# Kernel optimization log

Measured on AMD Instinct MI355X. Metric: run time of the kernel, lower is better.

The kernel has to match this reference:

```python
import jax, jax.numpy as jnp
import numpy as np

D_MODEL = 512
D_INNER = 1024   # expand=2
D_STATE = 16
D_CONV = 4
DT_RANK = 32     # ceil(d_model/16)
N_LAYERS = 3
STATE_DIM = 256
NUM_ACTIONS = 9
BATCH = 8
SEQ = 1024


def setup_inputs() -> dict:
    key = jax.random.key(0)
    ks = iter(jax.random.split(key, 32))
    def nrm(shape, scale=0.02):
        return jax.random.normal(next(ks), shape, jnp.float32) * scale
    inp = {}
    inp["state_sequences"] = jax.random.normal(next(ks), (BATCH, SEQ, STATE_DIM), jnp.float32)
    inp["embed_w"] = nrm((D_MODEL, STATE_DIM), STATE_DIM ** -0.5)
    inp["embed_b"] = jnp.zeros((D_MODEL,), jnp.float32)
    inp["in_proj_w"] = nrm((N_LAYERS, 2 * D_INNER, D_MODEL), D_MODEL ** -0.5)
    inp["conv_w"] = nrm((N_LAYERS, D_INNER, D_CONV), 0.2)
    inp["conv_b"] = jnp.zeros((N_LAYERS, D_INNER), jnp.float32)
    inp["x_proj_w"] = nrm((N_LAYERS, DT_RANK + 2 * D_STATE, D_INNER), D_INNER ** -0.5)
    inp["dt_proj_w"] = nrm((N_LAYERS, D_INNER, DT_RANK), DT_RANK ** -0.5)
    # bias so that softplus(dt) ~ 0.01 (standard mamba dt init)
    inp["dt_proj_b"] = jnp.full((N_LAYERS, D_INNER), float(np.log(np.expm1(0.01))), jnp.float32)
    # S4D-real init: A_n = n for n = 1..d_state
    inp["A_log"] = jnp.log(jnp.broadcast_to(
        jnp.arange(1, D_STATE + 1, dtype=jnp.float32), (N_LAYERS, D_INNER, D_STATE)))
    inp["D"] = jnp.ones((N_LAYERS, D_INNER), jnp.float32)
    inp["out_proj_w"] = nrm((N_LAYERS, D_MODEL, D_INNER), D_INNER ** -0.5)
    inp["head1_w"] = nrm((D_MODEL // 2, D_MODEL), D_MODEL ** -0.5)
    inp["head1_b"] = jnp.zeros((D_MODEL // 2,), jnp.float32)
    inp["head2_w"] = nrm((NUM_ACTIONS, D_MODEL // 2), (D_MODEL // 2) ** -0.5)
    inp["head2_b"] = jnp.zeros((NUM_ACTIONS,), jnp.float32)
    return inp


def _mamba_block(x, in_w, cw, cb, xw, dtw, dtb, A_log, Dp, ow):
    """One mamba-ssm Mamba layer (d_inner=2*d_model, d_state=16, d_conv=4)."""
    B, L, _ = x.shape
    xz = jnp.einsum('bld,ed->ble', x, in_w)            # (B,L,2*d_inner)
    xi, z = jnp.split(xz, 2, axis=-1)
    # causal depthwise conv1d along time
    xc = jnp.pad(xi, ((0, 0), (D_CONV - 1, 0), (0, 0)))
    conv = jax.lax.conv_general_dilated(
        xc.transpose(0, 2, 1), cw[:, None, :], (1,), 'VALID',
        feature_group_count=D_INNER)                   # (B,d_inner,L)
    xi = jax.nn.silu(conv.transpose(0, 2, 1) + cb)     # (B,L,d_inner)
    dbl = jnp.einsum('bld,ed->ble', xi, xw)            # (B,L,dt_rank+2*d_state)
    dt, Bm, Cm = jnp.split(dbl, [DT_RANK, DT_RANK + D_STATE], axis=-1)
    dt = jax.nn.softplus(jnp.einsum('blr,dr->bld', dt, dtw) + dtb)  # (B,L,d_inner)
    A = -jnp.exp(A_log)                                # (d_inner,d_state)

    def step(h, inputs):
        dt_t, x_t, B_t, C_t = inputs                   # (B,di),(B,di),(B,ds),(B,ds)
        dA = jnp.exp(dt_t[:, :, None] * A)             # (B,di,ds)
        h = dA * h + (dt_t * x_t)[:, :, None] * B_t[:, None, :]
        y_t = jnp.einsum('bds,bs->bd', h, C_t)
        return h, y_t

    h0 = jnp.zeros((B, D_INNER, D_STATE), xi.dtype)
    seq = (dt.transpose(1, 0, 2), xi.transpose(1, 0, 2),
           Bm.transpose(1, 0, 2), Cm.transpose(1, 0, 2))
    _, ys = jax.lax.scan(step, h0, seq)                # (L,B,d_inner)
    y = ys.transpose(1, 0, 2) + xi * Dp
    y = y * jax.nn.silu(z)
    return jnp.einsum('bld,ed->ble', y, ow)            # (B,L,d_model)


def reference(state_sequences, embed_w, embed_b, in_proj_w, conv_w, conv_b,
              x_proj_w, dt_proj_w, dt_proj_b, A_log, D, out_proj_w,
              head1_w, head1_b, head2_w, head2_b):
    x = jnp.einsum('bls,ds->bld', state_sequences, embed_w) + embed_b
    for i in range(N_LAYERS):
        x = _mamba_block(x, in_proj_w[i], conv_w[i], conv_b[i], x_proj_w[i],
                         dt_proj_w[i], dt_proj_b[i], A_log[i], D[i], out_proj_w[i])
    h = jax.nn.relu(jnp.einsum('bd,hd->bh', x[:, -1, :], head1_w) + head1_b)
    logits = jnp.einsum('bh,ah->ba', h, head2_w) + head2_b  # (B,num_actions)
    return logits
```

## Files before the change

### kernel.cpp

```cpp
#include <hip/hip_runtime.h>
#include <cstdint>
#include <cstddef>


#define DEVI static __device__ __forceinline__

using short8 = __attribute__((ext_vector_type(8))) short;
using f32x4  = __attribute__((ext_vector_type(4))) float;
typedef unsigned short ushort;
typedef unsigned int uint;

DEVI float sigmoidf_(float x) { return 1.f / (1.f + __expf(-x)); }
DEVI float siluf_(float x)    { return x * sigmoidf_(x); }
DEVI float softplusf_(float x){ return fmaxf(x, 0.f) + log1pf(expf(-fabsf(x))); }

DEVI ushort rne_bf16(float f) {
    uint u = __float_as_uint(f);
    return (ushort)((u + 0x7fffu + ((u >> 16) & 1u)) >> 16);
}
DEVI float bf16_to_f(ushort h) { return __uint_as_float(((uint)h) << 16); }

constexpr int LC = 32;
constexpr int NC = 32;
constexpr int PF = 8;

DEVI void cvt4(const float4 v, ushort* h, ushort* l) {
    const float vv[4] = {v.x, v.y, v.z, v.w};
    #pragma unroll
    for (int e = 0; e < 4; e++) {
        const ushort hh = rne_bf16(vv[e]);
        h[e] = hh;
        l[e] = rne_bf16(vv[e] - bf16_to_f(hh));
    }
}

__global__ __launch_bounds__(256)
void wcvt_kernel(const float* __restrict__ src, ushort* __restrict__ hi,
                 ushort* __restrict__ lo, int n4)
{
    const int idx = blockIdx.x * 256 + threadIdx.x;
    if (idx >= n4) return;
    const float4 v = reinterpret_cast<const float4*>(src)[idx];
    ushort h[4], l[4];
    cvt4(v, h, l);
    *reinterpret_cast<ushort4*>(&hi[idx * 4]) = make_ushort4(h[0], h[1], h[2], h[3]);
    *reinterpret_cast<ushort4*>(&lo[idx * 4]) = make_ushort4(l[0], l[1], l[2], l[3]);
}

__global__ __launch_bounds__(256)
void wcvt3_kernel(const float* __restrict__ s_in, const float* __restrict__ s_out,
                  const float* __restrict__ s_xp, ushort* __restrict__ dst)
{
    const int idx = blockIdx.x * 256 + threadIdx.x;
    if (idx >= 409600) return;
    const int e0 = idx * 4;
    const float* src; ushort* hb; ushort* lb; int loc;
    if (e0 < 1048576)      { src = s_in;  hb = dst;           lb = dst + 1048576; loc = e0; }
    else if (e0 < 1572864) { src = s_out; hb = dst + 2097152; lb = dst + 2621440; loc = e0 - 1048576; }
    else                   { src = s_xp;  hb = dst + 3145728; lb = dst + 3211264; loc = e0 - 1572864; }
    const float4 v = *reinterpret_cast<const float4*>(&src[loc]);
    ushort h[4], l[4];
    cvt4(v, h, l);
    *reinterpret_cast<ushort4*>(&hb[loc]) = make_ushort4(h[0], h[1], h[2], h[3]);
    *reinterpret_cast<ushort4*>(&lb[loc]) = make_ushort4(l[0], l[1], l[2], l[3]);
}

template<int ACT>
__global__ __launch_bounds__(256)
void gemm_mfma(const float* __restrict__ A, int lda,
               const ushort* __restrict__ Whi, const ushort* __restrict__ Wlo,
               int ldw, const float* __restrict__ bias,
               float* __restrict__ C, int ldc, int K)
{
    __shared__ short As_hi[4096], As_lo[4096], Ws_hi[4096], Ws_lo[4096];

    const int tid  = threadIdx.x;
    const int lane = tid & 63;
    const int wave = tid >> 6;
    const int wr   = wave >> 1;
    const int wc   = wave & 1;
    const int row0 = blockIdx.y * 128;
    const int col0 = blockIdx.x * 128;

    const int g  = tid & 3;
    const int r0 = tid >> 2;

    const int lg = lane >> 4;
    const int lm = lane & 15;
    const int chA = lg * 128 + ((wr * 64 + lm) ^ lg);
    const int chB = lg * 128 + ((wc * 64 + lm) ^ lg);

    f32x4 acc[4][4];
    #pragma unroll
    for (int i = 0; i < 4; i++)
        #pragma unroll
        for (int j = 0; j < 4; j++) acc[i][j] = (f32x4){0.f, 0.f, 0.f, 0.f};

    float4 av0[2], av1[2];
    short8 wh[2], wl8[2];

    auto gload = [&](int k0) {
        #pragma unroll
        for (int p = 0; p < 2; p++) {
            const int rr = r0 + p * 64;
            const float* ap = A + (size_t)(row0 + rr) * lda + k0 + g * 8;
            av0[p] = *reinterpret_cast<const float4*>(ap);
            av1[p] = *reinterpret_cast<const float4*>(ap + 4);
            const size_t wo = (size_t)(col0 + rr) * ldw + k0 + g * 8;
            wh[p]  = *reinterpret_cast<const short8*>(&Whi[wo]);
            wl8[p] = *reinterpret_cast<const short8*>(&Wlo[wo]);
        }
    };

    gload(0);

    for (int k0 = 0; k0 < K; k0 += 32) {
        #pragma unroll
        for (int p = 0; p < 2; p++) {
            const int ch = g * 128 + ((r0 + p * 64) ^ g);
            ushort h[8], l[8];
            cvt4(av0[p], h, l);
            cvt4(av1[p], h + 4, l + 4);
            short8 h8, l8;
            #pragma unroll
            for (int e = 0; e < 8; e++) { h8[e] = (short)h[e]; l8[e] = (short)l[e]; }
            *reinterpret_cast<short8*>(&As_hi[ch * 8]) = h8;
            *reinterpret_cast<short8*>(&As_lo[ch * 8]) = l8;
            *reinterpret_cast<short8*>(&Ws_hi[ch * 8]) = wh[p];
            *reinterpret_cast<short8*>(&Ws_lo[ch * 8]) = wl8[p];
        }
        if (k0 + 32 < K) gload(k0 + 32);
        __syncthreads();

        short8 a_hi[4], a_lo[4], b_hi[4], b_lo[4];
        #pragma unroll
        for (int i = 0; i < 4; i++) {
            a_hi[i] = *reinterpret_cast<const short8*>(&As_hi[(chA + i * 16) * 8]);
            a_lo[i] = *reinterpret_cast<const short8*>(&As_lo[(chA + i * 16) * 8]);
        }
        #pragma unroll
        for (int j = 0; j < 4; j++) {
            b_hi[j] = *reinterpret_cast<const short8*>(&Ws_hi[(chB + j * 16) * 8]);
            b_lo[j] = *reinterpret_cast<const short8*>(&Ws_lo[(chB + j * 16) * 8]);
        }
        #pragma unroll
        for (int i = 0; i < 4; i++)
            #pragma unroll
            for (int j = 0; j < 4; j++) {
                acc[i][j] = __builtin_amdgcn_mfma_f32_16x16x32_bf16(a_hi[i], b_hi[j], acc[i][j], 0, 0, 0);
                acc[i][j] = __builtin_amdgcn_mfma_f32_16x16x32_bf16(a_hi[i], b_lo[j], acc[i][j], 0, 0, 0);
                acc[i][j] = __builtin_amdgcn_mfma_f32_16x16x32_bf16(a_lo[i], b_hi[j], acc[i][j], 0, 0, 0);
            }
        __syncthreads();
    }

    #pragma unroll
    for (int i = 0; i < 4; i++) {
        const int grow = row0 + wr * 64 + i * 16 + lg * 4;
        #pragma unroll
        for (int j = 0; j < 4; j++) {
            const int gcol = col0 + wc * 64 + j * 16 + lm;
            float bv = 0.f;
            if constexpr (ACT >= 1) bv = bias[gcol];
            #pragma unroll
            for (int r = 0; r < 4; r++)
                C[(size_t)(grow + r) * ldc + gcol] = acc[i][j][r] + bv;
        }
    }
}

__global__ __launch_bounds__(256)
void gemm_mfma_xp(const float* __restrict__ A,
                  const ushort* __restrict__ Whi,
                  const ushort* __restrict__ Wlo,
                  float* __restrict__ P)
{
    __shared__ short As_hi[2048], As_lo[2048], Ws_hi[2048], Ws_lo[2048];

    const int tid  = threadIdx.x;
    const int lane = tid & 63;
    const int wave = tid >> 6;
    const int wr   = wave >> 1;
    const int wc   = wave & 1;
    const int row0 = blockIdx.x * 64;
    const int kp   = blockIdx.y;

    const int g = tid & 3;
    const int r = tid >> 2;
    const int ch_st = g * 64 + (r ^ g);

    const int lg = lane >> 4;
    const int lm = lane & 15;

    f32x4 acc[2][2];
    #pragma unroll
    for (int i = 0; i < 2; i++)
        #pragma unroll
        for (int j = 0; j < 2; j++) acc[i][j] = (f32x4){0.f, 0.f, 0.f, 0.f};

    for (int ks = 0; ks < 4; ks++) {
        const int kbase = kp * 128 + ks * 32;
        __syncthreads();
        {
            const float* ap = A + (size_t)(row0 + r) * 1024 + kbase + g * 8;
            const float4 v0 = *reinterpret_cast<const float4*>(ap);
            const float4 v1 = *reinterpret_cast<const float4*>(ap + 4);
            ushort h[8], l[8];
            cvt4(v0, h, l);
            cvt4(v1, h + 4, l + 4);
            short8 h8, l8;
            #pragma unroll
            for (int e = 0; e < 8; e++) { h8[e] = (short)h[e]; l8[e] = (short)l[e]; }
            *reinterpret_cast<short8*>(&As_hi[ch_st * 8]) = h8;
            *reinterpret_cast<short8*>(&As_lo[ch_st * 8]) = l8;
        }
        {
            const size_t wo = (size_t)r * 1024 + kbase + g * 8;
            *reinterpret_cast<short8*>(&Ws_hi[ch_st * 8]) =
                *reinterpret_cast<const short8*>(&Whi[wo]);
            *reinterpret_cast<short8*>(&Ws_lo[ch_st * 8]) =
                *reinterpret_cast<const short8*>(&Wlo[wo]);
        }
        __syncthreads();

        short8 a_hi[2], a_lo[2], b_hi[2], b_lo[2];
        #pragma unroll
        for (int i = 0; i < 2; i++) {
            const int ch = lg * 64 + ((wr * 32 + i * 16 + lm) ^ lg);
            a_hi[i] = *reinterpret_cast<const short8*>(&As_hi[ch * 8]);
            a_lo[i] = *reinterpret_cast<const short8*>(&As_lo[ch * 8]);
        }
        #pragma unroll
        for (int j = 0; j < 2; j++) {
            const int ch = lg * 64 + ((wc * 32 + j * 16 + lm) ^ lg);
            b_hi[j] = *reinterpret_cast<const short8*>(&Ws_hi[ch * 8]);
            b_lo[j] = *reinterpret_cast<const short8*>(&Ws_lo[ch * 8]);
        }
        #pragma unroll
        for (int i = 0; i < 2; i++)
            #pragma unroll
            for (int j = 0; j < 2; j++) {
                acc[i][j] = __builtin_amdgcn_mfma_f32_16x16x32_bf16(a_hi[i], b_hi[j], acc[i][j], 0, 0, 0);
                acc[i][j] = __builtin_amdgcn_mfma_f32_16x16x32_bf16(a_hi[i], b_lo[j], acc[i][j], 0, 0, 0);
                acc[i][j] = __builtin_amdgcn_mfma_f32_16x16x32_bf16(a_lo[i], b_hi[j], acc[i][j], 0, 0, 0);
            }
    }

    #pragma unroll
    for (int i = 0; i < 2; i++) {
        const int grow = row0 + wr * 32 + i * 16 + lg * 4;
        #pragma unroll
        for (int j = 0; j < 2; j++) {
            const int gcol = wc * 32 + j * 16 + lm;
            #pragma unroll
            for (int rr = 0; rr < 4; rr++)
                P[((size_t)kp * 8192 + grow + rr) * 64 + gcol] = acc[i][j][rr];
        }
    }
}

__global__ __launch_bounds__(256)
void xp_reduce(const float* __restrict__ P, float* __restrict__ dbl)
{
    const int idx = blockIdx.x * 256 + threadIdx.x;
    float s = 0.f;
    #pragma unroll
    for (int p = 0; p < 8; p++) s += P[(size_t)p * 524288 + idx];
    dbl[idx] = s;
}

__global__ __launch_bounds__(256)
void conv_silu_kernel(const float* __restrict__ xz,
                      const float* __restrict__ cw,
                      const float* __restrict__ cb,
                      float* __restrict__ xi)
{
    const int idx = blockIdx.x * 256 + threadIdx.x;
    const int d = idx & 1023;
    const int l = (idx >> 10) & 1023;
    const int b = idx >> 20;

    const float4 w = reinterpret_cast<const float4*>(cw)[d];
    float acc = cb[d];
    const float* base = xz + (size_t)b * 1024 * 2048 + d;
    if (l >= 3) acc = fmaf(base[(size_t)(l - 3) * 2048], w.x, acc);
    if (l >= 2) acc = fmaf(base[(size_t)(l - 2) * 2048], w.y, acc);
    if (l >= 1) acc = fmaf(base[(size_t)(l - 1) * 2048], w.z, acc);
    acc = fmaf(base[(size_t)l * 2048], w.w, acc);
    xi[idx] = siluf_(acc);
}

__global__ __launch_bounds__(256)
void dt_kernel(const float* __restrict__ dbl,
               const float* __restrict__ dtw,
               const float* __restrict__ dtb,
               float* __restrict__ dtout)
{
    __shared__ float S[LC][32];
    const int tid = threadIdx.x;
    const int d   = blockIdx.x * 256 + tid;
    const int c   = blockIdx.y;
    const int b   = blockIdx.z;
    const int t0  = c * LC;

    {
        const int t = tid >> 3, q = tid & 7;
        *reinterpret_cast<float4*>(&S[t][q * 4]) =
            *reinterpret_cast<const float4*>(&dbl[((size_t)b * 1024 + t0 + t) * 64 + q * 4]);
    }
    __syncthreads();

    float W[32];
    #pragma unroll
    for (int q = 0; q < 8; q++)
        *reinterpret_cast<float4*>(&W[q * 4]) =
            *reinterpret_cast<const float4*>(&dtw[(size_t)d * 32 + q * 4]);
    const float bias = dtb[d];

    float* dto = dtout + ((size_t)b * 1024 + t0) * 1024 + d;
    #pragma unroll 4
    for (int t = 0; t < LC; t++) {
        float a0 = bias, a1 = 0.f, a2 = 0.f, a3 = 0.f;
        #pragma unroll
        for (int q = 0; q < 8; q += 4) {
            const float4 s0 = *reinterpret_cast<const float4*>(&S[t][q * 4]);
            const float4 s1 = *reinterpret_cast<const float4*>(&S[t][q * 4 + 4]);
            a0 = fmaf(W[q*4+0], s0.x, a0); a1 = fmaf(W[q*4+1], s0.y, a1);
            a2 = fmaf(W[q*4+2], s0.z, a2); a3 = fmaf(W[q*4+3], s0.w, a3);
            a0 = fmaf(W[q*4+4], s1.x, a0); a1 = fmaf(W[q*4+5], s1.y, a1);
            a2 = fmaf(W[q*4+6], s1.z, a2); a3 = fmaf(W[q*4+7], s1.w, a3);
        }
        dto[(size_t)t * 1024] = softplusf_((a0 + a1) + (a2 + a3));
    }
}

__global__ __launch_bounds__(256)
void scan_p1(const float* __restrict__ xi,
             const float* __restrict__ dtin,
             const float* __restrict__ dbl,
             const float* __restrict__ A_log,
             float* __restrict__ hend,
             float* __restrict__ dtsum)
{
    __shared__ float S[LC][16];
    const int tid = threadIdx.x;
    const int d   = blockIdx.x * 256 + tid;
    const int c   = blockIdx.y;
    const int b   = blockIdx.z;
    const int t0  = c * LC;

    if (tid < 128) {
        const int t = tid >> 2, q = tid & 3;
        *reinterpret_cast<float4*>(&S[t][q * 4]) =
            *reinterpret_cast<const float4*>(&dbl[((size_t)b * 1024 + t0 + t) * 64 + 32 + q * 4]);
    }
    __syncthreads();

    float A[16], h[16];
    #pragma unroll
    for (int s = 0; s < 16; s++) A[s] = -__expf(A_log[d * 16 + s]);
    #pragma unroll
    for (int s = 0; s < 16; s++) h[s] = 0.f;
    float dts = 0.f;

    const float* xi_p = xi   + ((size_t)b * 1024 + t0) * 1024 + d;
    const float* dt_p = dtin + ((size_t)b * 1024 + t0) * 1024 + d;

    float xA[PF], xB[PF], dA[PF], dB[PF];
    #pragma unroll
    for (int j = 0; j < PF; j++) {
        xA[j] = xi_p[(size_t)j * 1024];
        dA[j] = dt_p[(size_t)j * 1024];
    }

    auto batch = [&](int bt, float (&cx)[PF], float (&cd)[PF],
                     float (&nx)[PF], float (&nd)[PF], bool pre) {
        if (pre) {
            #pragma unroll
            for (int j = 0; j < PF; j++) {
                const size_t tt = (size_t)((bt + 1) * PF + j);
                nx[j] = xi_p[tt * 1024];
                nd[j] = dt_p[tt * 1024];
            }
        }
        #pragma unroll
        for (int j = 0; j < PF; j++) {
            const int t = bt * PF + j;
            const float dtv = cd[j];
            dts += dtv;
            const float dx = dtv * cx[j];
            #pragma unroll
            for (int q = 0; q < 4; q++) {
                const float4 Bv = *reinterpret_cast<const float4*>(&S[t][q * 4]);
                h[q*4+0] = fmaf(__expf(dtv * A[q*4+0]), h[q*4+0], dx * Bv.x);
                h[q*4+1] = fmaf(__expf(dtv * A[q*4+1]), h[q*4+1], dx * Bv.y);
                h[q*4+2] = fmaf(__expf(dtv * A[q*4+2]), h[q*4+2], dx * Bv.z);
                h[q*4+3] = fmaf(__expf(dtv * A[q*4+3]), h[q*4+3], dx * Bv.w);
            }
        }
    };
    batch(0, xA, dA, xB, dB, true);
    batch(1, xB, dB, xA, dA, true);
    batch(2, xA, dA, xB, dB, true);
    batch(3, xB, dB, xA, dA, false);

    float* hp = hend + (((size_t)b * NC + c) * 1024 + d) * 16;
    #pragma unroll
    for (int s = 0; s < 16; s += 4)
        *reinterpret_cast<float4*>(&hp[s]) = *reinterpret_cast<const float4*>(&h[s]);
    dtsum[((size_t)b * NC + c) * 1024 + d] = dts;
}

__global__ __launch_bounds__(256)
void scan_p2(float* __restrict__ hbuf,
             const float* __restrict__ dtsum,
             const float* __restrict__ A_log)
{
    const int gid = blockIdx.x * 256 + threadIdx.x;
    const int s = gid & 15;
    const int d = (gid >> 4) & 1023;
    const int b = gid >> 14;

    const float A = -__expf(A_log[d * 16 + s]);
    float h = 0.f;
    #pragma unroll
    for (int c = 0; c < NC; c++) {
        const size_t idx = (((size_t)b * NC + c) * 1024 + d) * 16 + s;
        const float he = hbuf[idx];
        const float aP = __expf(A * dtsum[((size_t)b * NC + c) * 1024 + d]);
        hbuf[idx] = h;
        h = fmaf(aP, h, he);
    }
}

__global__ __launch_bounds__(256)
void scan_p3(const float* __restrict__ xi,
             const float* __restrict__ dtin,
             const float* __restrict__ dbl,
             float* __restrict__ xz,
             const float* __restrict__ A_log,
             const float* __restrict__ Dp,
             const float* __restrict__ h0)
{
    __shared__ float S[LC][32];
    const int tid = threadIdx.x;
    const int d   = blockIdx.x * 256 + tid;
    const int c   = blockIdx.y;
    const int b   = blockIdx.z;
    const int t0  = c * LC;

    {
        const int t = tid >> 3, q = tid & 7;
        *reinterpret_cast<float4*>(&S[t][q * 4]) =
            *reinterpret_cast<const float4*>(&dbl[((size_t)b * 1024 + t0 + t) * 64 + 32 + q * 4]);
    }
    __syncthreads();

    float A[16], h[16];
    #pragma unroll
    for (int s = 0; s < 16; s++) A[s] = -__expf(A_log[d * 16 + s]);
    const float* h0p = h0 + (((size_t)b * NC + c) * 1024 + d) * 16;
    #pragma unroll
    for (int s = 0; s < 16; s += 4)
        *reinterpret_cast<float4*>(&h[s]) = *reinterpret_cast<const float4*>(&h0p[s]);

    const float Dv = Dp[d];
    const float* xi_p = xi   + ((size_t)b * 1024 + t0) * 1024 + d;
    const float* dt_p = dtin + ((size_t)b * 1024 + t0) * 1024 + d;
    const float* z_p  = xz   + ((size_t)b * 1024 + t0) * 2048 + 1024 + d;
    float*       y_p  = xz   + ((size_t)b * 1024 + t0) * 2048 + d;

    float xA[PF], xB[PF], zA[PF], zB[PF], dA[PF], dB[PF];
    #pragma unroll
    for (int j = 0; j < PF; j++) {
        xA[j] = xi_p[(size_t)j * 1024];
        zA[j] = z_p[(size_t)j * 2048];
        dA[j] = dt_p[(size_t)j * 1024];
    }

    auto batch = [&](int bt, float (&cx)[PF], float (&cz)[PF], float (&cd)[PF],
                     float (&nx)[PF], float (&nz)[PF], float (&nd)[PF], bool pre) {
        if (pre) {
            #pragma unroll
            for (int j = 0; j < PF; j++) {
                const size_t tt = (size_t)((bt + 1) * PF + j);
                nx[j] = xi_p[tt * 1024];
                nz[j] = z_p[tt * 2048];
                nd[j] = dt_p[tt * 1024];
            }
        }
        #pragma unroll
        for (int j = 0; j < PF; j++) {
            const int t = bt * PF + j;
            const float dtv = cd[j];
            const float dx  = dtv * cx[j];
            float y = 0.f;
            #pragma unroll
            for (int q = 0; q < 4; q++) {
                const float4 Bv = *reinterpret_cast<const float4*>(&S[t][q * 4]);
                const float4 Cv = *reinterpret_cast<const float4*>(&S[t][16 + q * 4]);
                h[q*4+0] = fmaf(__expf(dtv * A[q*4+0]), h[q*4+0], dx * Bv.x);
                h[q*4+1] = fmaf(__expf(dtv * A[q*4+1]), h[q*4+1], dx * Bv.y);
                h[q*4+2] = fmaf(__expf(dtv * A[q*4+2]), h[q*4+2], dx * Bv.z);
                h[q*4+3] = fmaf(__expf(dtv * A[q*4+3]), h[q*4+3], dx * Bv.w);
                y = fmaf(h[q*4+0], Cv.x, y);
                y = fmaf(h[q*4+1], Cv.y, y);
                y = fmaf(h[q*4+2], Cv.z, y);
                y = fmaf(h[q*4+3], Cv.w, y);
            }
            y_p[(size_t)t * 2048] = (y + cx[j] * Dv) * siluf_(cz[j]);
        }
    };
    batch(0, xA, zA, dA, xB, zB, dB, true);
    batch(1, xB, zB, dB, xA, zA, dA, true);
    batch(2, xA, zA, dA, xB, zB, dB, true);
    batch(3, xB, zB, dB, xA, zA, dA, false);
}

__global__ __launch_bounds__(256)
void head1_kernel(const float* __restrict__ x,
                  const float* __restrict__ w,
                  const float* __restrict__ bias,
                  float* __restrict__ hh)
{
    const int tid = threadIdx.x;
    const int jl  = tid >> 4;
    const int ks  = tid & 15;
    const int j   = blockIdx.x * 16 + jl;

    const float* wr = w + (size_t)j * 512 + ks * 32;
    float acc[8];
    #pragma unroll
    for (int b = 0; b < 8; b++) {
        const float* xr = x + ((size_t)b * 1024 + 1023) * 512 + ks * 32;
        float a = 0.f;
        #pragma unroll
        for (int k = 0; k < 32; k += 4) {
            const float4 wv = *reinterpret_cast<const float4*>(&wr[k]);
            const float4 xv = *reinterpret_cast<const float4*>(&xr[k]);
            a = fmaf(wv.x, xv.x, a); a = fmaf(wv.y, xv.y, a);
            a = fmaf(wv.z, xv.z, a); a = fmaf(wv.w, xv.w, a);
        }
        acc[b] = a;
    }
    #pragma unroll
    for (int b = 0; b < 8; b++) {
        float p = acc[b];
        p += __shfl_xor(p, 1);
        p += __shfl_xor(p, 2);
        p += __shfl_xor(p, 4);
        p += __shfl_xor(p, 8);
        if (ks == 0) hh[b * 256 + j] = fmaxf(p + bias[j], 0.f);
    }
}

__global__ void head2_kernel(const float* __restrict__ hh,
                             const float* __restrict__ w,
                             const float* __restrict__ b2,
                             float* __restrict__ out)
{
    const int t = threadIdx.x;
    if (t < 72) {
        const int bb = t / 9, a = t % 9;
        const float* hr = hh + bb * 256;
        const float* wr = w + a * 256;
        float acc = b2[a];
        for (int jj = 0; jj < 256; jj++) acc = fmaf(hr[jj], wr[jj], acc);
        out[t] = acc;
    }
}


extern "C" void kernel_launch(void* const* d_in, const int* in_sizes, int n_in,
                              void* d_out, int out_size, void* d_ws, size_t ws_size,
                              hipStream_t stream)
{
    const float* state     = (const float*)d_in[0];
    const float* embed_w   = (const float*)d_in[1];
    const float* embed_b   = (const float*)d_in[2];
    const float* in_proj_w = (const float*)d_in[3];
    const float* conv_w    = (const float*)d_in[4];
    const float* conv_b    = (const float*)d_in[5];
    const float* x_proj_w  = (const float*)d_in[6];
    const float* dt_proj_w = (const float*)d_in[7];
    const float* dt_proj_b = (const float*)d_in[8];
    const float* A_log     = (const float*)d_in[9];
    const float* Dp        = (const float*)d_in[10];
    const float* out_proj_w= (const float*)d_in[11];
    const float* h1w       = (const float*)d_in[12];
    const float* h1b       = (const float*)d_in[13];
    const float* h2w       = (const float*)d_in[14];
    const float* h2b       = (const float*)d_in[15];
    float* out = (float*)d_out;

    float* x    = (float*)d_ws;
    float* xz   = x    + (size_t)8192 * 512;
    float* xi   = xz   + (size_t)8192 * 2048;
    float* dtbf = xi   + (size_t)8192 * 1024;
    float* dbl  = dtbf + (size_t)8192 * 1024;
    float* hh   = dbl  + (size_t)8192 * 64;
    ushort* wl = (ushort*)(hh + 2048);
    ushort* we_hi = wl + 3276800;
    ushort* we_lo = we_hi + 131072;
    float* dtsum = (float*)(we_lo + 131072);

    float* dblp = x;
    float* hbuf = x;

    const dim3 blk(256);

    wcvt_kernel<<<dim3(128), blk, 0, stream>>>(embed_w, we_hi, we_lo, 131072 / 4);
    gemm_mfma<1><<<dim3(4, 64), blk, 0, stream>>>(
        state, 256, we_hi, we_lo, 256, embed_b, x, 512, 256);

    for (int i = 0; i < 3; i++) {
        const float* Alog_i = A_log + (size_t)i * 1024 * 16;
        const float* dtw_i  = dt_proj_w + (size_t)i * 1024 * 32;
        const float* dtb_i  = dt_proj_b + (size_t)i * 1024;

        wcvt3_kernel<<<dim3(1600), blk, 0, stream>>>(
            in_proj_w + (size_t)i * 2048 * 512,
            out_proj_w + (size_t)i * 512 * 1024,
            x_proj_w + (size_t)i * 64 * 1024, wl);

        gemm_mfma<0><<<dim3(16, 64), blk, 0, stream>>>(
            x, 512, wl, wl + 1048576, 512, nullptr, xz, 2048, 512);

        conv_silu_kernel<<<dim3(8 * 1024 * 1024 / 256), blk, 0, stream>>>(
            xz, conv_w + (size_t)i * 1024 * 4, conv_b + (size_t)i * 1024, xi);

        gemm_mfma_xp<<<dim3(128, 8), blk, 0, stream>>>(
            xi, wl + 3145728, wl + 3211264, dblp);
        xp_reduce<<<dim3(2048), blk, 0, stream>>>(dblp, dbl);

        dt_kernel<<<dim3(4, NC, 8), blk, 0, stream>>>(dbl, dtw_i, dtb_i, dtbf);

        scan_p1<<<dim3(4, NC, 8), blk, 0, stream>>>(
            xi, dtbf, dbl, Alog_i, hbuf, dtsum);
        scan_p2<<<dim3(512), blk, 0, stream>>>(hbuf, dtsum, Alog_i);
        scan_p3<<<dim3(4, NC, 8), blk, 0, stream>>>(
            xi, dtbf, dbl, xz, Alog_i, Dp + (size_t)i * 1024, hbuf);

        gemm_mfma<0><<<dim3(4, 64), blk, 0, stream>>>(
            xz, 2048, wl + 2097152, wl + 2621440, 1024, nullptr, x, 512, 1024);
    }

    head1_kernel<<<dim3(16), blk, 0, stream>>>(x, h1w, h1b, hh);
    head2_kernel<<<dim3(1), dim3(128), 0, stream>>>(hh, h2w, h2b, out);
}
```

Baseline: 834.9 us.

## Emit pre-split bf16 hi/lo activations from producers to skip GEMM-side conversion

Producers of the GEMM A operands (the embed GEMM, the out_proj GEMM and scan_p3) now write activations directly as bf16 hi/lo pairs instead of fp32. The consuming GEMMs load these split halves straight into shared memory and no longer run the per-tile fp32-to-bf16x2 conversion. Global traffic stays about the same size but the conversion ALU work is removed from the GEMM main loops. The head kernel is adapted to rebuild fp32 from the hi/lo pair. Buffer aliasing changes, with y stored inside the xz rows using a stride of 4096.

```diff
diff --git a/kernel.cpp b/kernel.cpp
--- a/kernel.cpp
+++ b/kernel.cpp
@@ -65,12 +65,15 @@
     *reinterpret_cast<ushort4*>(&lb[loc]) = make_ushort4(l[0], l[1], l[2], l[3]);
 }
 
-template<int ACT>
-__global__ __launch_bounds__(256)
-void gemm_mfma(const float* __restrict__ A, int lda,
+template<int ACT, bool ASPLIT, bool OSPLIT>
+__global__ __launch_bounds__(256)
+void gemm_mfma(const float* __restrict__ A,
+               const ushort* __restrict__ Ahi, const ushort* __restrict__ Alo,
+               int lda,
                const ushort* __restrict__ Whi, const ushort* __restrict__ Wlo,
                int ldw, const float* __restrict__ bias,
-               float* __restrict__ C, int ldc, int K)
+               float* __restrict__ C, ushort* __restrict__ Chi,
+               ushort* __restrict__ Clo, int ldc, int K)
 {
     __shared__ short As_hi[4096], As_lo[4096], Ws_hi[4096], Ws_lo[4096];
 
@@ -97,15 +100,21 @@
         for (int j = 0; j < 4; j++) acc[i][j] = (f32x4){0.f, 0.f, 0.f, 0.f};
 
     float4 av0[2], av1[2];
-    short8 wh[2], wl8[2];
+    short8 ah[2], al[2], wh[2], wl8[2];
 
     auto gload = [&](int k0) {
         #pragma unroll
         for (int p = 0; p < 2; p++) {
             const int rr = r0 + p * 64;
-            const float* ap = A + (size_t)(row0 + rr) * lda + k0 + g * 8;
-            av0[p] = *reinterpret_cast<const float4*>(ap);
-            av1[p] = *reinterpret_cast<const float4*>(ap + 4);
+            if constexpr (ASPLIT) {
+                const size_t ao = (size_t)(row0 + rr) * lda + k0 + g * 8;
+                ah[p] = *reinterpret_cast<const short8*>(&Ahi[ao]);
+                al[p] = *reinterpret_cast<const short8*>(&Alo[ao]);
+            } else {
+                const float* ap = A + (size_t)(row0 + rr) * lda + k0 + g * 8;
+                av0[p] = *reinterpret_cast<const float4*>(ap);
+                av1[p] = *reinterpret_cast<const float4*>(ap + 4);
+            }
             const size_t wo = (size_t)(col0 + rr) * ldw + k0 + g * 8;
             wh[p]  = *reinterpret_cast<const short8*>(&Whi[wo]);
             wl8[p] = *reinterpret_cast<const short8*>(&Wlo[wo]);
@@ -118,14 +127,19 @@
         #pragma unroll
         for (int p = 0; p < 2; p++) {
             const int ch = g * 128 + ((r0 + p * 64) ^ g);
-            ushort h[8], l[8];
-            cvt4(av0[p], h, l);
-            cvt4(av1[p], h + 4, l + 4);
-            short8 h8, l8;
-            #pragma unroll
-            for (int e = 0; e < 8; e++) { h8[e] = (short)h[e]; l8[e] = (short)l[e]; }
-            *reinterpret_cast<short8*>(&As_hi[ch * 8]) = h8;
-            *reinterpret_cast<short8*>(&As_lo[ch * 8]) = l8;
+            if constexpr (ASPLIT) {
+                *reinterpret_cast<short8*>(&As_hi[ch * 8]) = ah[p];
+                *reinterpret_cast<short8*>(&As_lo[ch * 8]) = al[p];
+            } else {
+                ushort h[8], l[8];
+                cvt4(av0[p], h, l);
+                cvt4(av1[p], h + 4, l + 4);
+                short8 h8, l8;
+                #pragma unroll
+                for (int e = 0; e < 8; e++) { h8[e] = (short)h[e]; l8[e] = (short)l[e]; }
+                *reinterpret_cast<short8*>(&As_hi[ch * 8]) = h8;
+                *reinterpret_cast<short8*>(&As_lo[ch * 8]) = l8;
+            }
             *reinterpret_cast<short8*>(&Ws_hi[ch * 8]) = wh[p];
             *reinterpret_cast<short8*>(&Ws_lo[ch * 8]) = wl8[p];
         }
@@ -163,8 +177,16 @@
             float bv = 0.f;
             if constexpr (ACT >= 1) bv = bias[gcol];
             #pragma unroll
-            for (int r = 0; r < 4; r++)
-                C[(size_t)(grow + r) * ldc + gcol] = acc[i][j][r] + bv;
+            for (int r = 0; r < 4; r++) {
+                const float v = acc[i][j][r] + bv;
+                if constexpr (OSPLIT) {
+                    const ushort hv = rne_bf16(v);
+                    Chi[(size_t)(grow + r) * ldc + gcol] = hv;
+                    Clo[(size_t)(grow + r) * ldc + gcol] = rne_bf16(v - bf16_to_f(hv));
+                } else {
+                    C[(size_t)(grow + r) * ldc + gcol] = v;
+                }
+            }
         }
     }
 }
@@ -468,7 +490,8 @@
     const float* xi_p = xi   + ((size_t)b * 1024 + t0) * 1024 + d;
     const float* dt_p = dtin + ((size_t)b * 1024 + t0) * 1024 + d;
     const float* z_p  = xz   + ((size_t)b * 1024 + t0) * 2048 + 1024 + d;
-    float*       y_p  = xz   + ((size_t)b * 1024 + t0) * 2048 + d;
+    ushort* yh_p = reinterpret_cast<ushort*>(xz + ((size_t)b * 1024 + t0) * 2048) + d;
+    ushort* yl_p = yh_p + 1024;
 
     float xA[PF], xB[PF], zA[PF], zB[PF], dA[PF], dB[PF];
     #pragma unroll
@@ -508,7 +531,10 @@
                 y = fmaf(h[q*4+2], Cv.z, y);
                 y = fmaf(h[q*4+3], Cv.w, y);
             }
-            y_p[(size_t)t * 2048] = (y + cx[j] * Dv) * siluf_(cz[j]);
+            const float yv = (y + cx[j] * Dv) * siluf_(cz[j]);
+            const ushort hv = rne_bf16(yv);
+            yh_p[(size_t)t * 4096] = hv;
+            yl_p[(size_t)t * 4096] = rne_bf16(yv - bf16_to_f(hv));
         }
     };
     batch(0, xA, zA, dA, xB, zB, dB, true);
@@ -518,7 +544,8 @@
 }
 
 __global__ __launch_bounds__(256)
-void head1_kernel(const float* __restrict__ x,
+void head1_kernel(const ushort* __restrict__ xh,
+                  const ushort* __restrict__ xl,
                   const float* __restrict__ w,
                   const float* __restrict__ bias,
                   float* __restrict__ hh)
@@ -532,14 +559,17 @@
     float acc[8];
     #pragma unroll
     for (int b = 0; b < 8; b++) {
-        const float* xr = x + ((size_t)b * 1024 + 1023) * 512 + ks * 32;
+        const size_t ro = ((size_t)b * 1024 + 1023) * 512 + ks * 32;
         float a = 0.f;
         #pragma unroll
         for (int k = 0; k < 32; k += 4) {
             const float4 wv = *reinterpret_cast<const float4*>(&wr[k]);
-            const float4 xv = *reinterpret_cast<const float4*>(&xr[k]);
-            a = fmaf(wv.x, xv.x, a); a = fmaf(wv.y, xv.y, a);
-            a = fmaf(wv.z, xv.z, a); a = fmaf(wv.w, xv.w, a);
+            const ushort4 hv = *reinterpret_cast<const ushort4*>(&xh[ro + k]);
+            const ushort4 lv = *reinterpret_cast<const ushort4*>(&xl[ro + k]);
+            a = fmaf(wv.x, bf16_to_f(hv.x) + bf16_to_f(lv.x), a);
+            a = fmaf(wv.y, bf16_to_f(hv.y) + bf16_to_f(lv.y), a);
+            a = fmaf(wv.z, bf16_to_f(hv.z) + bf16_to_f(lv.z), a);
+            a = fmaf(wv.w, bf16_to_f(hv.w) + bf16_to_f(lv.w), a);
         }
         acc[b] = a;
     }
@@ -593,8 +623,13 @@
     const float* h2b       = (const float*)d_in[15];
     float* out = (float*)d_out;
 
-    float* x    = (float*)d_ws;
-    float* xz   = x    + (size_t)8192 * 512;
+    float* reg0 = (float*)d_ws;
+    ushort* xh  = (ushort*)reg0;
+    ushort* xl  = xh + (size_t)8192 * 512;
+    float* dblp = reg0;
+    float* hbuf = reg0;
+
+    float* xz   = reg0 + (size_t)8192 * 512;
     float* xi   = xz   + (size_t)8192 * 2048;
     float* dtbf = xi   + (size_t)8192 * 1024;
     float* dbl  = dtbf + (size_t)8192 * 1024;
@@ -604,14 +639,15 @@
     ushort* we_lo = we_hi + 131072;
     float* dtsum = (float*)(we_lo + 131072);
 
-    float* dblp = x;
-    float* hbuf = x;
+    ushort* yh = (ushort*)xz;
+    ushort* yl = (ushort*)xz + 1024;
 
     const dim3 blk(256);
 
     wcvt_kernel<<<dim3(128), blk, 0, stream>>>(embed_w, we_hi, we_lo, 131072 / 4);
-    gemm_mfma<1><<<dim3(4, 64), blk, 0, stream>>>(
-        state, 256, we_hi, we_lo, 256, embed_b, x, 512, 256);
+    gemm_mfma<1, false, true><<<dim3(4, 64), blk, 0, stream>>>(
+        state, nullptr, nullptr, 256, we_hi, we_lo, 256, embed_b,
+        nullptr, xh, xl, 512, 256);
 
     for (int i = 0; i < 3; i++) {
         const float* Alog_i = A_log + (size_t)i * 1024 * 16;
@@ -623,8 +659,9 @@
             out_proj_w + (size_t)i * 512 * 1024,
             x_proj_w + (size_t)i * 64 * 1024, wl);
 
-        gemm_mfma<0><<<dim3(16, 64), blk, 0, stream>>>(
-            x, 512, wl, wl + 1048576, 512, nullptr, xz, 2048, 512);
+        gemm_mfma<0, true, false><<<dim3(16, 64), blk, 0, stream>>>(
+            nullptr, xh, xl, 512, wl, wl + 1048576, 512, nullptr,
+            xz, nullptr, nullptr, 2048, 512);
 
         conv_silu_kernel<<<dim3(8 * 1024 * 1024 / 256), blk, 0, stream>>>(
             xz, conv_w + (size_t)i * 1024 * 4, conv_b + (size_t)i * 1024, xi);
@@ -641,10 +678,11 @@
         scan_p3<<<dim3(4, NC, 8), blk, 0, stream>>>(
             xi, dtbf, dbl, xz, Alog_i, Dp + (size_t)i * 1024, hbuf);
 
-        gemm_mfma<0><<<dim3(4, 64), blk, 0, stream>>>(
-            xz, 2048, wl + 2097152, wl + 2621440, 1024, nullptr, x, 512, 1024);
-    }
-
-    head1_kernel<<<dim3(16), blk, 0, stream>>>(x, h1w, h1b, hh);
+        gemm_mfma<0, true, true><<<dim3(4, 64), blk, 0, stream>>>(
+            nullptr, yh, yl, 4096, wl + 2097152, wl + 2621440, 1024, nullptr,
+            nullptr, xh, xl, 512, 1024);
+    }
+
+    head1_kernel<<<dim3(16), blk, 0, stream>>>(xh, xl, h1w, h1b, hh);
     head2_kernel<<<dim3(1), dim3(128), 0, stream>>>(hh, h2w, h2b, out);
 }
```

New measurement: 907.8 us. 8.7% more time.
